# Performance work log

Hardware: AMD Instinct MI355X
Metric: run time of the kernel (lower is better)

The kernel has to match this reference:

```python
import jax, jax.numpy as jnp
import numpy as np

QUERY_INDS = (0, 1, 2, 3)
HEADS = 8
HEAD_DIM = 64
SCALE = HEAD_DIM ** -0.5
DIM = 512
INNER = HEADS * HEAD_DIM  # 512


def setup_inputs() -> dict:
    key = jax.random.key(0)
    ks = jax.random.split(key, 6)
    B, N = 4, 2048
    x = jax.random.normal(ks[0], (B, N, DIM), dtype=jnp.float32)
    bias = jax.random.normal(ks[1], (B, HEADS, N, N), dtype=jnp.float32)
    # weights stored as (in, out); math-equivalent to torch Linear
    Wq = jax.random.normal(ks[2], (DIM, INNER), dtype=jnp.float32) * (DIM ** -0.5)
    Wkv = jax.random.normal(ks[3], (DIM, 2 * INNER), dtype=jnp.float32) * (DIM ** -0.5)
    Wo = jax.random.normal(ks[4], (INNER, DIM), dtype=jnp.float32) * (INNER ** -0.5)
    bo = jax.random.normal(ks[5], (DIM,), dtype=jnp.float32) * 0.01
    return {"x": x, "bias": bias, "Wq": Wq, "Wkv": Wkv, "Wo": Wo, "bo": bo}


def _split_heads(t):
    # (B, n, H*d) -> (B, H, n, d)
    B, n, _ = t.shape
    return t.reshape(B, n, HEADS, HEAD_DIM).transpose(0, 2, 1, 3)


def reference(x, bias, Wq, Wkv, Wo, bo):
    qi = jnp.array(QUERY_INDS)
    q = _split_heads(x[:, qi] @ Wq)          # (B, H, M, d), M = len(QUERY_INDS)
    kv = x @ Wkv                              # (B, N, 2*inner)
    k, v = jnp.split(kv, 2, axis=-1)
    k = _split_heads(k)                       # (B, H, N, d)
    v = _split_heads(v)                       # (B, H, N, d)
    dots = jnp.einsum('bhmd,bhnd->bhmn', q, k) * SCALE
    dots = dots + bias[:, :, qi]              # gather bias rows at query positions
    attn = jax.nn.softmax(dots, axis=-1)      # dropout=0 (eval)
    out = jnp.einsum('bhmn,bhnd->bhmd', attn, v)
    B, _, M, _ = out.shape
    out = out.transpose(0, 2, 1, 3).reshape(B, M, INNER)  # (B, M, H*d)
    return out @ Wo + bo
```

## Files before the change

### kernel.cpp

```cpp
#include <hip/hip_runtime.h>
#include <stddef.h>

#define B_ 4
#define N_ 2048
#define C_ 512
#define H_ 8
#define D_ 64
#define M_ 4
#define HM_ 32
#define SCALE_ 0.125f

#define QK_OFF   0
#define DOTS_OFF 65536
#define AXP_OFF  (65536 + 524288)
#define Q_OFF    1114112
#define OV_OFF   1122304

__global__ __launch_bounds__(256) void zero_kernel(float* __restrict__ wsz, float* __restrict__ out) {
    int idx = blockIdx.x * 256 + threadIdx.x;
    if (idx < 16384) wsz[idx] = 0.f;
    else out[idx - 16384] = 0.f;
}

__global__ __launch_bounds__(256) void k1a_q(const float* __restrict__ x, const float* __restrict__ Wq,
                                             float* __restrict__ q_ws) {
    __shared__ float W[64][68];
    __shared__ float xr[16][68];
    int t = threadIdx.x;
    int c0 = blockIdx.x * 64, j0 = blockIdx.y * 64;
    #pragma unroll
    for (int i = 0; i < 4; i++) {
        int f = t + i * 256; int cc = f >> 4, j4 = f & 15;
        *(float4*)&W[cc][j4 * 4] = *(const float4*)&Wq[(size_t)(c0 + cc) * 512 + j0 + j4 * 4];
    }
    {
        int r = t >> 4, c4 = t & 15;
        int b = r >> 2, m = r & 3;
        *(float4*)&xr[r][c4 * 4] = *(const float4*)&x[((size_t)(b * N_) + m) * C_ + c0 + c4 * 4];
    }
    __syncthreads();
    int j = t & 63, rg = t >> 6;
    float acc[4] = {0, 0, 0, 0};
    #pragma unroll 16
    for (int cc = 0; cc < 64; cc++) {
        float w = W[cc][j];
        #pragma unroll
        for (int i = 0; i < 4; i++) acc[i] += xr[rg * 4 + i][cc] * w;
    }
    #pragma unroll
    for (int i = 0; i < 4; i++) {
        int r = rg * 4 + i;
        atomicAdd(&q_ws[r * 512 + j0 + j], acc[i]);
    }
}

__global__ __launch_bounds__(256) void k1b_qk(const float* __restrict__ Wkv, const float* __restrict__ q_ws,
                                              float* __restrict__ qk_ws) {
    __shared__ float WkT[64][68];
    __shared__ float qh[16][68];
    int t = threadIdx.x;
    int c0 = blockIdx.x * 64; int h = blockIdx.y;
    #pragma unroll
    for (int i = 0; i < 4; i++) {
        int f = t + i * 256; int cc = f >> 4, d4 = f & 15;
        float4 v = *(const float4*)&Wkv[(size_t)(c0 + cc) * 1024 + h * 64 + d4 * 4];
        WkT[d4 * 4 + 0][cc] = v.x; WkT[d4 * 4 + 1][cc] = v.y;
        WkT[d4 * 4 + 2][cc] = v.z; WkT[d4 * 4 + 3][cc] = v.w;
    }
    {
        int r = t >> 4, d4 = t & 15;
        *(float4*)&qh[r][d4 * 4] = *(const float4*)&q_ws[r * 512 + h * 64 + d4 * 4];
    }
    __syncthreads();
    int c = t & 63, rg = t >> 6;
    float acc[4] = {0, 0, 0, 0};
    #pragma unroll 16
    for (int d = 0; d < 64; d++) {
        float w = WkT[d][c];
        #pragma unroll
        for (int i = 0; i < 4; i++) acc[i] += qh[rg * 4 + i][d] * w;
    }
    #pragma unroll
    for (int i = 0; i < 4; i++) {
        int r = rg * 4 + i; int b = r >> 2, m = r & 3;
        qk_ws[((size_t)(b * HM_) + h * M_ + m) * 512 + c0 + c] = acc[i] * SCALE_;
    }
}

__global__ __launch_bounds__(256) void k2_dots(const float* __restrict__ x, const float* __restrict__ qk_ws,
                                               float* __restrict__ dots) {
    __shared__ float xt[64][66];
    __shared__ float qT[64][36];
    int t = threadIdx.x;
    int n0 = blockIdx.x * 64; int b = blockIdx.y; int ks = blockIdx.z;
    int p = t & 31, qg = t >> 5;
    float acc[2][4] = {{0, 0, 0, 0}, {0, 0, 0, 0}};
    for (int ch = 0; ch < 4; ch++) {
        int c0 = ks * 256 + ch * 64;
        #pragma unroll
        for (int i = 0; i < 4; i++) {
            int f = t + i * 256; int n = f >> 4, c4 = f & 15;
            float4 v = *(const float4*)&x[((size_t)(b * N_) + n0 + n) * C_ + c0 + c4 * 4];
            xt[c4 * 4 + 0][n] = v.x; xt[c4 * 4 + 1][n] = v.y;
            xt[c4 * 4 + 2][n] = v.z; xt[c4 * 4 + 3][n] = v.w;
        }
        #pragma unroll
        for (int i = 0; i < 2; i++) {
            int f = t + i * 256; int hm = f >> 4, c4 = f & 15;
            float4 v = *(const float4*)&qk_ws[((size_t)(b * HM_) + hm) * 512 + c0 + c4 * 4];
            qT[c4 * 4 + 0][hm] = v.x; qT[c4 * 4 + 1][hm] = v.y;
            qT[c4 * 4 + 2][hm] = v.z; qT[c4 * 4 + 3][hm] = v.w;
        }
        __syncthreads();
        #pragma unroll 16
        for (int kk = 0; kk < 64; kk++) {
            float2 xv = *(const float2*)&xt[kk][p * 2];
            float4 qv = *(const float4*)&qT[kk][qg * 4];
            acc[0][0] += qv.x * xv.x; acc[1][0] += qv.x * xv.y;
            acc[0][1] += qv.y * xv.x; acc[1][1] += qv.y * xv.y;
            acc[0][2] += qv.z * xv.x; acc[1][2] += qv.z * xv.y;
            acc[0][3] += qv.w * xv.x; acc[1][3] += qv.w * xv.y;
        }
        __syncthreads();
    }
    #pragma unroll
    for (int i = 0; i < 4; i++) {
        int hm = qg * 4 + i;
        *(float2*)&dots[(size_t)ks * 262144 + ((size_t)(b * HM_) + hm) * N_ + n0 + p * 2] =
            make_float2(acc[0][i], acc[1][i]);
    }
}

__global__ __launch_bounds__(256) void k3_softmax(const float* __restrict__ bias, float* __restrict__ dots) {
    __shared__ float red[256];
    int t = threadIdx.x;
    int row = blockIdx.x;
    int b = row >> 5, hm = row & 31, h = hm >> 2, m = hm & 3;
    const float* dA = dots + (size_t)row * N_;
    const float* dB = dots + 262144 + (size_t)row * N_;
    const float* brow = bias + ((size_t)(b * H_ + h) * N_ + m) * N_;
    float v[8];
    float mx = -1e30f;
    #pragma unroll
    for (int i = 0; i < 8; i++) {
        int n = t + i * 256;
        v[i] = dA[n] + dB[n] + brow[n];
        mx = fmaxf(mx, v[i]);
    }
    red[t] = mx; __syncthreads();
    for (int s = 128; s > 0; s >>= 1) { if (t < s) red[t] = fmaxf(red[t], red[t + s]); __syncthreads(); }
    mx = red[0]; __syncthreads();
    float ssum = 0.f;
    #pragma unroll
    for (int i = 0; i < 8; i++) { v[i] = __expf(v[i] - mx); ssum += v[i]; }
    red[t] = ssum; __syncthreads();
    for (int s = 128; s > 0; s >>= 1) { if (t < s) red[t] += red[t + s]; __syncthreads(); }
    float inv = 1.0f / red[0];
    float* aw = dots + (size_t)row * N_;
    #pragma unroll
    for (int i = 0; i < 8; i++) aw[t + i * 256] = v[i] * inv;
}

__global__ __launch_bounds__(256) void k4_attnx(const float* __restrict__ x, const float* __restrict__ attn,
                                                float* __restrict__ axp) {
    __shared__ float xn[64][68];
    __shared__ float at[64][36];
    int t = threadIdx.x;
    int c0 = blockIdx.x * 64; int s = blockIdx.y; int b = blockIdx.z;
    int p = t & 31, qg = t >> 5;
    float acc[2][4] = {{0, 0, 0, 0}, {0, 0, 0, 0}};
    for (int sub = 0; sub < 4; sub++) {
        int n0 = s * 256 + sub * 64;
        #pragma unroll
        for (int i = 0; i < 4; i++) {
            int f = t + i * 256; int nn = f >> 4, c4 = f & 15;
            *(float4*)&xn[nn][c4 * 4] =
                *(const float4*)&x[((size_t)(b * N_) + n0 + nn) * C_ + c0 + c4 * 4];
        }
        #pragma unroll
        for (int i = 0; i < 2; i++) {
            int f = t + i * 256; int hm = f >> 4, n4 = f & 15;
            float4 v = *(const float4*)&attn[((size_t)(b * HM_) + hm) * N_ + n0 + n4 * 4];
            at[n4 * 4 + 0][hm] = v.x; at[n4 * 4 + 1][hm] = v.y;
            at[n4 * 4 + 2][hm] = v.z; at[n4 * 4 + 3][hm] = v.w;
        }
        __syncthreads();
        #pragma unroll 16
        for (int nn = 0; nn < 64; nn++) {
            float2 xv = *(const float2*)&xn[nn][p * 2];
            float4 av = *(const float4*)&at[nn][qg * 4];
            acc[0][0] += av.x * xv.x; acc[1][0] += av.x * xv.y;
            acc[0][1] += av.y * xv.x; acc[1][1] += av.y * xv.y;
            acc[0][2] += av.z * xv.x; acc[1][2] += av.z * xv.y;
            acc[0][3] += av.w * xv.x; acc[1][3] += av.w * xv.y;
        }
        __syncthreads();
    }
    #pragma unroll
    for (int i = 0; i < 4; i++) {
        int hm = qg * 4 + i;
        *(float2*)&axp[(((size_t)(s * B_) + b) * HM_ + hm) * C_ + c0 + p * 2] =
            make_float2(acc[0][i], acc[1][i]);
    }
}

__global__ __launch_bounds__(256) void k5a_ov(const float* __restrict__ Wkv, const float* __restrict__ axp,
                                              float* __restrict__ ov_ws) {
    __shared__ float Wv[64][68];
    __shared__ float axh[16][68];
    int t = threadIdx.x;
    int c0 = blockIdx.x * 64; int h = blockIdx.y;
    #pragma unroll
    for (int i = 0; i < 4; i++) {
        int f = t + i * 256; int cc = f >> 4, e4 = f & 15;
        *(float4*)&Wv[cc][e4 * 4] =
            *(const float4*)&Wkv[(size_t)(c0 + cc) * 1024 + 512 + h * 64 + e4 * 4];
    }
    {
        int r = t >> 4, c4 = t & 15;
        int b = r >> 2, m = r & 3;
        float4 a = make_float4(0, 0, 0, 0);
        #pragma unroll
        for (int s = 0; s < 8; s++) {
            float4 v = *(const float4*)&axp[(((size_t)(s * B_) + b) * HM_ + h * M_ + m) * C_ + c0 + c4 * 4];
            a.x += v.x; a.y += v.y; a.z += v.z; a.w += v.w;
        }
        *(float4*)&axh[r][c4 * 4] = a;
    }
    __syncthreads();
    int e = t & 63, rg = t >> 6;
    float acc[4] = {0, 0, 0, 0};
    #pragma unroll 16
    for (int cc = 0; cc < 64; cc++) {
        float w = Wv[cc][e];
        #pragma unroll
        for (int i = 0; i < 4; i++) acc[i] += axh[rg * 4 + i][cc] * w;
    }
    #pragma unroll
    for (int i = 0; i < 4; i++) {
        int r = rg * 4 + i;
        atomicAdd(&ov_ws[r * 512 + h * 64 + e], acc[i]);
    }
}

__global__ __launch_bounds__(256) void k5b_out(const float* __restrict__ Wo, const float* __restrict__ bo,
                                               const float* __restrict__ ov_ws, float* __restrict__ out) {
    __shared__ float W[64][68];
    __shared__ float ovr[16][68];
    int t = threadIdx.x;
    int i0 = blockIdx.x * 64; int j0 = blockIdx.y * 64;
    #pragma unroll
    for (int i = 0; i < 4; i++) {
        int f = t + i * 256; int ii = f >> 4, j4 = f & 15;
        *(float4*)&W[ii][j4 * 4] = *(const float4*)&Wo[(size_t)(i0 + ii) * 512 + j0 + j4 * 4];
    }
    {
        int r = t >> 4, c4 = t & 15;
        *(float4*)&ovr[r][c4 * 4] = *(const float4*)&ov_ws[r * 512 + i0 + c4 * 4];
    }
    __syncthreads();
    int j = t & 63, rg = t >> 6;
    float binit = (blockIdx.x == 0) ? bo[j0 + j] : 0.f;
    float acc[4] = {binit, binit, binit, binit};
    #pragma unroll 16
    for (int ii = 0; ii < 64; ii++) {
        float w = W[ii][j];
        #pragma unroll
        for (int i = 0; i < 4; i++) acc[i] += ovr[rg * 4 + i][ii] * w;
    }
    #pragma unroll
    for (int i = 0; i < 4; i++) {
        int r = rg * 4 + i;
        atomicAdd(&out[r * 512 + j0 + j], acc[i]);
    }
}

extern "C" void kernel_launch(void* const* d_in, const int* in_sizes, int n_in,
                              void* d_out, int out_size, void* d_ws, size_t ws_size,
                              hipStream_t stream) {
    const float* x    = (const float*)d_in[0];
    const float* bias = (const float*)d_in[1];
    const float* Wq   = (const float*)d_in[2];
    const float* Wkv  = (const float*)d_in[3];
    const float* Wo   = (const float*)d_in[4];
    const float* bo   = (const float*)d_in[5];
    float* out = (float*)d_out;
    float* ws  = (float*)d_ws;

    float* qk_ws = ws + QK_OFF;
    float* dots  = ws + DOTS_OFF;
    float* axp   = ws + AXP_OFF;
    float* q_ws  = ws + Q_OFF;
    float* ov_ws = ws + OV_OFF;

    zero_kernel<<<96, 256, 0, stream>>>(q_ws, out);
    k1a_q<<<dim3(8, 8), 256, 0, stream>>>(x, Wq, q_ws);
    k1b_qk<<<dim3(8, 8), 256, 0, stream>>>(Wkv, q_ws, qk_ws);
    k2_dots<<<dim3(32, 4, 2), 256, 0, stream>>>(x, qk_ws, dots);
    k3_softmax<<<128, 256, 0, stream>>>(bias, dots);
    k4_attnx<<<dim3(8, 8, 4), 256, 0, stream>>>(x, dots, axp);
    k5a_ov<<<dim3(8, 8), 256, 0, stream>>>(Wkv, axp, ov_ws);
    k5b_out<<<dim3(8, 8), 256, 0, stream>>>(Wo, bo, ov_ws, out);
}
```

Before: 622.1 us.

## Enlarge register tiles to 4x4 in dots and attn-x kernels with finer split-K

The dots and attention-times-x kernels now give each thread a 4x4 output tile instead of 2x4, reading float4 from shared memory with wider 128-column tiles. The reduction dimension is split into more partitions (4 channel splits for dots, 16 sequence splits for attn-x) so the block count stays the same. Softmax and the output projection are updated to sum the extra partial buffers, and the workspace offsets grow to hold them. The goal is more FMAs per shared-memory load in these two GEMM-like stages, paid for with extra partial-sum traffic and larger workspace.

```diff
diff --git a/kernel.cpp b/kernel.cpp
--- a/kernel.cpp
+++ b/kernel.cpp
@@ -12,9 +12,9 @@
 
 #define QK_OFF   0
 #define DOTS_OFF 65536
-#define AXP_OFF  (65536 + 524288)
-#define Q_OFF    1114112
-#define OV_OFF   1122304
+#define AXP_OFF  (65536 + 1048576)
+#define Q_OFF    (65536 + 1048576 + 1048576)
+#define OV_OFF   (Q_OFF + 8192)
 
 __global__ __launch_bounds__(256) void zero_kernel(float* __restrict__ wsz, float* __restrict__ out) {
     int idx = blockIdx.x * 256 + threadIdx.x;
@@ -89,45 +89,47 @@
 
 __global__ __launch_bounds__(256) void k2_dots(const float* __restrict__ x, const float* __restrict__ qk_ws,
                                                float* __restrict__ dots) {
-    __shared__ float xt[64][66];
-    __shared__ float qT[64][36];
-    int t = threadIdx.x;
-    int n0 = blockIdx.x * 64; int b = blockIdx.y; int ks = blockIdx.z;
-    int p = t & 31, qg = t >> 5;
-    float acc[2][4] = {{0, 0, 0, 0}, {0, 0, 0, 0}};
-    for (int ch = 0; ch < 4; ch++) {
-        int c0 = ks * 256 + ch * 64;
-        #pragma unroll
-        for (int i = 0; i < 4; i++) {
-            int f = t + i * 256; int n = f >> 4, c4 = f & 15;
-            float4 v = *(const float4*)&x[((size_t)(b * N_) + n0 + n) * C_ + c0 + c4 * 4];
-            xt[c4 * 4 + 0][n] = v.x; xt[c4 * 4 + 1][n] = v.y;
-            xt[c4 * 4 + 2][n] = v.z; xt[c4 * 4 + 3][n] = v.w;
+    __shared__ __align__(16) float xt[64][132];
+    __shared__ __align__(16) float qT[64][36];
+    int t = threadIdx.x;
+    int n0 = blockIdx.x * 128; int b = blockIdx.y; int ks = blockIdx.z;
+    int p = t & 31, g = t >> 5;
+    float acc[4][4] = {{0,0,0,0},{0,0,0,0},{0,0,0,0},{0,0,0,0}};
+    for (int ch = 0; ch < 2; ch++) {
+        int cs = ks * 128 + ch * 64;
+        #pragma unroll
+        for (int it = 0; it < 8; it++) {
+            int cc = (t & 15) + 16 * (it & 3);
+            int q  = (t >> 4) + 16 * (it >> 2);
+            const float* gp = &x[((size_t)(b * N_) + n0 + 4 * q) * C_ + cs + cc];
+            float4 v;
+            v.x = gp[0]; v.y = gp[C_]; v.z = gp[2 * C_]; v.w = gp[3 * C_];
+            *(float4*)&xt[cc][4 * q] = v;
         }
         #pragma unroll
         for (int i = 0; i < 2; i++) {
             int f = t + i * 256; int hm = f >> 4, c4 = f & 15;
-            float4 v = *(const float4*)&qk_ws[((size_t)(b * HM_) + hm) * 512 + c0 + c4 * 4];
+            float4 v = *(const float4*)&qk_ws[((size_t)(b * HM_) + hm) * 512 + cs + c4 * 4];
             qT[c4 * 4 + 0][hm] = v.x; qT[c4 * 4 + 1][hm] = v.y;
             qT[c4 * 4 + 2][hm] = v.z; qT[c4 * 4 + 3][hm] = v.w;
         }
         __syncthreads();
-        #pragma unroll 16
+        #pragma unroll 8
         for (int kk = 0; kk < 64; kk++) {
-            float2 xv = *(const float2*)&xt[kk][p * 2];
-            float4 qv = *(const float4*)&qT[kk][qg * 4];
-            acc[0][0] += qv.x * xv.x; acc[1][0] += qv.x * xv.y;
-            acc[0][1] += qv.y * xv.x; acc[1][1] += qv.y * xv.y;
-            acc[0][2] += qv.z * xv.x; acc[1][2] += qv.z * xv.y;
-            acc[0][3] += qv.w * xv.x; acc[1][3] += qv.w * xv.y;
+            float4 xv = *(const float4*)&xt[kk][p * 4];
+            float4 qv = *(const float4*)&qT[kk][g * 4];
+            acc[0][0] += qv.x * xv.x; acc[0][1] += qv.x * xv.y; acc[0][2] += qv.x * xv.z; acc[0][3] += qv.x * xv.w;
+            acc[1][0] += qv.y * xv.x; acc[1][1] += qv.y * xv.y; acc[1][2] += qv.y * xv.z; acc[1][3] += qv.y * xv.w;
+            acc[2][0] += qv.z * xv.x; acc[2][1] += qv.z * xv.y; acc[2][2] += qv.z * xv.z; acc[2][3] += qv.z * xv.w;
+            acc[3][0] += qv.w * xv.x; acc[3][1] += qv.w * xv.y; acc[3][2] += qv.w * xv.z; acc[3][3] += qv.w * xv.w;
         }
         __syncthreads();
     }
     #pragma unroll
     for (int i = 0; i < 4; i++) {
-        int hm = qg * 4 + i;
-        *(float2*)&dots[(size_t)ks * 262144 + ((size_t)(b * HM_) + hm) * N_ + n0 + p * 2] =
-            make_float2(acc[0][i], acc[1][i]);
+        int hm = g * 4 + i;
+        *(float4*)&dots[(size_t)ks * 262144 + ((size_t)(b * HM_) + hm) * N_ + n0 + p * 4] =
+            make_float4(acc[i][0], acc[i][1], acc[i][2], acc[i][3]);
     }
 }
 
@@ -136,15 +138,17 @@
     int t = threadIdx.x;
     int row = blockIdx.x;
     int b = row >> 5, hm = row & 31, h = hm >> 2, m = hm & 3;
-    const float* dA = dots + (size_t)row * N_;
-    const float* dB = dots + 262144 + (size_t)row * N_;
+    const float* d0 = dots + (size_t)row * N_;
+    const float* d1 = dots + 262144 + (size_t)row * N_;
+    const float* d2 = dots + 524288 + (size_t)row * N_;
+    const float* d3 = dots + 786432 + (size_t)row * N_;
     const float* brow = bias + ((size_t)(b * H_ + h) * N_ + m) * N_;
     float v[8];
     float mx = -1e30f;
     #pragma unroll
     for (int i = 0; i < 8; i++) {
         int n = t + i * 256;
-        v[i] = dA[n] + dB[n] + brow[n];
+        v[i] = d0[n] + d1[n] + d2[n] + d3[n] + brow[n];
         mx = fmaxf(mx, v[i]);
     }
     red[t] = mx; __syncthreads();
@@ -163,19 +167,19 @@
 
 __global__ __launch_bounds__(256) void k4_attnx(const float* __restrict__ x, const float* __restrict__ attn,
                                                 float* __restrict__ axp) {
-    __shared__ float xn[64][68];
-    __shared__ float at[64][36];
-    int t = threadIdx.x;
-    int c0 = blockIdx.x * 64; int s = blockIdx.y; int b = blockIdx.z;
-    int p = t & 31, qg = t >> 5;
-    float acc[2][4] = {{0, 0, 0, 0}, {0, 0, 0, 0}};
-    for (int sub = 0; sub < 4; sub++) {
-        int n0 = s * 256 + sub * 64;
-        #pragma unroll
-        for (int i = 0; i < 4; i++) {
-            int f = t + i * 256; int nn = f >> 4, c4 = f & 15;
-            *(float4*)&xn[nn][c4 * 4] =
-                *(const float4*)&x[((size_t)(b * N_) + n0 + nn) * C_ + c0 + c4 * 4];
+    __shared__ __align__(16) float xn[64][132];
+    __shared__ __align__(16) float at[64][36];
+    int t = threadIdx.x;
+    int c0 = blockIdx.x * 128; int s = blockIdx.y; int b = blockIdx.z;
+    int p = t & 31, g = t >> 5;
+    float acc[4][4] = {{0,0,0,0},{0,0,0,0},{0,0,0,0},{0,0,0,0}};
+    for (int sub = 0; sub < 2; sub++) {
+        int n0 = s * 128 + sub * 64;
+        #pragma unroll
+        for (int i = 0; i < 8; i++) {
+            int f = t + i * 256; int nn = f >> 5, c8 = f & 31;
+            *(float4*)&xn[nn][c8 * 4] =
+                *(const float4*)&x[((size_t)(b * N_) + n0 + nn) * C_ + c0 + c8 * 4];
         }
         #pragma unroll
         for (int i = 0; i < 2; i++) {
@@ -185,22 +189,22 @@
             at[n4 * 4 + 2][hm] = v.z; at[n4 * 4 + 3][hm] = v.w;
         }
         __syncthreads();
-        #pragma unroll 16
+        #pragma unroll 8
         for (int nn = 0; nn < 64; nn++) {
-            float2 xv = *(const float2*)&xn[nn][p * 2];
-            float4 av = *(const float4*)&at[nn][qg * 4];
-            acc[0][0] += av.x * xv.x; acc[1][0] += av.x * xv.y;
-            acc[0][1] += av.y * xv.x; acc[1][1] += av.y * xv.y;
-            acc[0][2] += av.z * xv.x; acc[1][2] += av.z * xv.y;
-            acc[0][3] += av.w * xv.x; acc[1][3] += av.w * xv.y;
+            float4 xv = *(const float4*)&xn[nn][p * 4];
+            float4 av = *(const float4*)&at[nn][g * 4];
+            acc[0][0] += av.x * xv.x; acc[0][1] += av.x * xv.y; acc[0][2] += av.x * xv.z; acc[0][3] += av.x * xv.w;
+            acc[1][0] += av.y * xv.x; acc[1][1] += av.y * xv.y; acc[1][2] += av.y * xv.z; acc[1][3] += av.y * xv.w;
+            acc[2][0] += av.z * xv.x; acc[2][1] += av.z * xv.y; acc[2][2] += av.z * xv.z; acc[2][3] += av.z * xv.w;
+            acc[3][0] += av.w * xv.x; acc[3][1] += av.w * xv.y; acc[3][2] += av.w * xv.z; acc[3][3] += av.w * xv.w;
         }
         __syncthreads();
     }
     #pragma unroll
     for (int i = 0; i < 4; i++) {
-        int hm = qg * 4 + i;
-        *(float2*)&axp[(((size_t)(s * B_) + b) * HM_ + hm) * C_ + c0 + p * 2] =
-            make_float2(acc[0][i], acc[1][i]);
+        int hm = g * 4 + i;
+        *(float4*)&axp[(((size_t)(s * B_) + b) * HM_ + hm) * C_ + c0 + p * 4] =
+            make_float4(acc[i][0], acc[i][1], acc[i][2], acc[i][3]);
     }
 }
 
@@ -221,7 +225,7 @@
         int b = r >> 2, m = r & 3;
         float4 a = make_float4(0, 0, 0, 0);
         #pragma unroll
-        for (int s = 0; s < 8; s++) {
+        for (int s = 0; s < 16; s++) {
             float4 v = *(const float4*)&axp[(((size_t)(s * B_) + b) * HM_ + h * M_ + m) * C_ + c0 + c4 * 4];
             a.x += v.x; a.y += v.y; a.z += v.z; a.w += v.w;
         }
@@ -296,9 +300,9 @@
     zero_kernel<<<96, 256, 0, stream>>>(q_ws, out);
     k1a_q<<<dim3(8, 8), 256, 0, stream>>>(x, Wq, q_ws);
     k1b_qk<<<dim3(8, 8), 256, 0, stream>>>(Wkv, q_ws, qk_ws);
-    k2_dots<<<dim3(32, 4, 2), 256, 0, stream>>>(x, qk_ws, dots);
+    k2_dots<<<dim3(16, 4, 4), 256, 0, stream>>>(x, qk_ws, dots);
     k3_softmax<<<128, 256, 0, stream>>>(bias, dots);
-    k4_attnx<<<dim3(8, 8, 4), 256, 0, stream>>>(x, dots, axp);
+    k4_attnx<<<dim3(4, 16, 4), 256, 0, stream>>>(x, dots, axp);
     k5a_ov<<<dim3(8, 8), 256, 0, stream>>>(Wkv, axp, ov_ws);
     k5b_out<<<dim3(8, 8), 256, 0, stream>>>(Wo, bo, ov_ws, out);
 }
```

Result: no change. 615.8 us (-1.0%).

## Fuse dots, softmax and attn-x into flash-style split-N kernel with partial reductions

Applied to the files above, without the earlier changes.

Merges the dots, softmax and attention-times-x kernels into one kernel. Each block handles 32 keys for one batch and keeps a local max and sum. The combine step moves into k5a_ov, which rescales 64 partial results with the merged max and sum. The atomicAdd accumulations and the separate zero kernel are replaced by partial-sum buffers reduced in the following kernel, and zeroing of out moves into k1b_qk. This removes the dots round trip through global memory and several launches, but grows the partial workspace to 64 splits and leaves k5a_ov with a serial 64-step reduction.

```diff
diff --git a/kernel.cpp b/kernel.cpp
--- a/kernel.cpp
+++ b/kernel.cpp
@@ -8,22 +8,18 @@
 #define D_ 64
 #define M_ 4
 #define HM_ 32
+#define S_ 64
 #define SCALE_ 0.125f
 
 #define QK_OFF   0
-#define DOTS_OFF 65536
-#define AXP_OFF  (65536 + 524288)
-#define Q_OFF    1114112
-#define OV_OFF   1122304
-
-__global__ __launch_bounds__(256) void zero_kernel(float* __restrict__ wsz, float* __restrict__ out) {
-    int idx = blockIdx.x * 256 + threadIdx.x;
-    if (idx < 16384) wsz[idx] = 0.f;
-    else out[idx - 16384] = 0.f;
-}
+#define PAX_OFF  65536
+#define MLOC_OFF (65536 + 4194304)
+#define LLOC_OFF (MLOC_OFF + 8192)
+#define QP_OFF   (LLOC_OFF + 8192)
+#define OVP_OFF  (QP_OFF + 65536)
 
 __global__ __launch_bounds__(256) void k1a_q(const float* __restrict__ x, const float* __restrict__ Wq,
-                                             float* __restrict__ q_ws) {
+                                             float* __restrict__ q_part) {
     __shared__ float W[64][68];
     __shared__ float xr[16][68];
     int t = threadIdx.x;
@@ -50,16 +46,18 @@
     #pragma unroll
     for (int i = 0; i < 4; i++) {
         int r = rg * 4 + i;
-        atomicAdd(&q_ws[r * 512 + j0 + j], acc[i]);
-    }
-}
-
-__global__ __launch_bounds__(256) void k1b_qk(const float* __restrict__ Wkv, const float* __restrict__ q_ws,
-                                              float* __restrict__ qk_ws) {
+        q_part[((size_t)blockIdx.x * 16 + r) * 512 + j0 + j] = acc[i];
+    }
+}
+
+__global__ __launch_bounds__(256) void k1b_qk(const float* __restrict__ Wkv, const float* __restrict__ q_part,
+                                              float* __restrict__ qk_ws, float* __restrict__ out) {
     __shared__ float WkT[64][68];
     __shared__ float qh[16][68];
     int t = threadIdx.x;
     int c0 = blockIdx.x * 64; int h = blockIdx.y;
+    int bid = blockIdx.y * 8 + blockIdx.x;
+    if (bid < 32) out[bid * 256 + t] = 0.f;
     #pragma unroll
     for (int i = 0; i < 4; i++) {
         int f = t + i * 256; int cc = f >> 4, d4 = f & 15;
@@ -69,7 +67,13 @@
     }
     {
         int r = t >> 4, d4 = t & 15;
-        *(float4*)&qh[r][d4 * 4] = *(const float4*)&q_ws[r * 512 + h * 64 + d4 * 4];
+        float4 a = make_float4(0.f, 0.f, 0.f, 0.f);
+        #pragma unroll
+        for (int cs = 0; cs < 8; cs++) {
+            float4 v = *(const float4*)&q_part[((size_t)cs * 16 + r) * 512 + h * 64 + d4 * 4];
+            a.x += v.x; a.y += v.y; a.z += v.z; a.w += v.w;
+        }
+        *(float4*)&qh[r][d4 * 4] = a;
     }
     __syncthreads();
     int c = t & 63, rg = t >> 6;
@@ -87,127 +91,170 @@
     }
 }
 
-__global__ __launch_bounds__(256) void k2_dots(const float* __restrict__ x, const float* __restrict__ qk_ws,
-                                               float* __restrict__ dots) {
-    __shared__ float xt[64][66];
-    __shared__ float qT[64][36];
-    int t = threadIdx.x;
-    int n0 = blockIdx.x * 64; int b = blockIdx.y; int ks = blockIdx.z;
-    int p = t & 31, qg = t >> 5;
-    float acc[2][4] = {{0, 0, 0, 0}, {0, 0, 0, 0}};
-    for (int ch = 0; ch < 4; ch++) {
-        int c0 = ks * 256 + ch * 64;
-        #pragma unroll
-        for (int i = 0; i < 4; i++) {
-            int f = t + i * 256; int n = f >> 4, c4 = f & 15;
-            float4 v = *(const float4*)&x[((size_t)(b * N_) + n0 + n) * C_ + c0 + c4 * 4];
-            xt[c4 * 4 + 0][n] = v.x; xt[c4 * 4 + 1][n] = v.y;
-            xt[c4 * 4 + 2][n] = v.z; xt[c4 * 4 + 3][n] = v.w;
-        }
-        #pragma unroll
-        for (int i = 0; i < 2; i++) {
-            int f = t + i * 256; int hm = f >> 4, c4 = f & 15;
-            float4 v = *(const float4*)&qk_ws[((size_t)(b * HM_) + hm) * 512 + c0 + c4 * 4];
-            qT[c4 * 4 + 0][hm] = v.x; qT[c4 * 4 + 1][hm] = v.y;
-            qT[c4 * 4 + 2][hm] = v.z; qT[c4 * 4 + 3][hm] = v.w;
-        }
-        __syncthreads();
-        #pragma unroll 16
-        for (int kk = 0; kk < 64; kk++) {
-            float2 xv = *(const float2*)&xt[kk][p * 2];
-            float4 qv = *(const float4*)&qT[kk][qg * 4];
-            acc[0][0] += qv.x * xv.x; acc[1][0] += qv.x * xv.y;
-            acc[0][1] += qv.y * xv.x; acc[1][1] += qv.y * xv.y;
-            acc[0][2] += qv.z * xv.x; acc[1][2] += qv.z * xv.y;
-            acc[0][3] += qv.w * xv.x; acc[1][3] += qv.w * xv.y;
-        }
-        __syncthreads();
-    }
-    #pragma unroll
-    for (int i = 0; i < 4; i++) {
-        int hm = qg * 4 + i;
-        *(float2*)&dots[(size_t)ks * 262144 + ((size_t)(b * HM_) + hm) * N_ + n0 + p * 2] =
-            make_float2(acc[0][i], acc[1][i]);
-    }
-}
-
-__global__ __launch_bounds__(256) void k3_softmax(const float* __restrict__ bias, float* __restrict__ dots) {
-    __shared__ float red[256];
-    int t = threadIdx.x;
-    int row = blockIdx.x;
-    int b = row >> 5, hm = row & 31, h = hm >> 2, m = hm & 3;
-    const float* dA = dots + (size_t)row * N_;
-    const float* dB = dots + 262144 + (size_t)row * N_;
-    const float* brow = bias + ((size_t)(b * H_ + h) * N_ + m) * N_;
-    float v[8];
-    float mx = -1e30f;
+__global__ __launch_bounds__(256) void k234_flash(const float* __restrict__ x, const float* __restrict__ qk_ws,
+                                                  const float* __restrict__ bias,
+                                                  float* __restrict__ pax, float* __restrict__ mloc,
+                                                  float* __restrict__ lloc) {
+    __shared__ __align__(16) float qk_s[32][516];
+    __shared__ __align__(16) float scratch[4][32][32];
+    __shared__ __align__(16) float dmat[32][36];
+    __shared__ __align__(16) float pT[32][36];
+    __shared__ float mrow[32];
+    __shared__ float red8[32][8];
+    int t = threadIdx.x;
+    int s = blockIdx.x, b = blockIdx.y;
+    int n0 = s * 32;
+
+    #pragma unroll
+    for (int k = 0; k < 16; k++) {
+        int idx = t + k * 256;
+        int row = idx >> 7, c4 = idx & 127;
+        *(float4*)&qk_s[row][c4 * 4] =
+            *(const float4*)&qk_ws[((size_t)(b * HM_) + row) * 512 + c4 * 4];
+    }
+    __syncthreads();
+
+    int hmg = t >> 6;
+    int ng  = (t >> 3) & 7;
+    int cs  = t & 7;
+    float d[8][4];
+    #pragma unroll
+    for (int i = 0; i < 8; i++)
+        #pragma unroll
+        for (int jn = 0; jn < 4; jn++) d[i][jn] = 0.f;
+
+    const float* xp = &x[((size_t)(b * N_) + n0 + ng * 4) * C_];
+    const float* qrow = &qk_s[hmg * 8][0];
+    #pragma unroll 2
+    for (int step = 0; step < 16; step++) {
+        int cbase = cs * 4 + step * 32;
+        float4 xv[4];
+        #pragma unroll
+        for (int jn = 0; jn < 4; jn++)
+            xv[jn] = *(const float4*)&xp[(size_t)jn * C_ + cbase];
+        #pragma unroll
+        for (int i = 0; i < 8; i++) {
+            float4 qv = *(const float4*)&qrow[i * 516 + cbase];
+            #pragma unroll
+            for (int jn = 0; jn < 4; jn++) {
+                d[i][jn] += qv.x * xv[jn].x + qv.y * xv[jn].y + qv.z * xv[jn].z + qv.w * xv[jn].w;
+            }
+        }
+    }
+    int pos = hmg * 8 + ng;
+    if (cs >= 4) {
+        #pragma unroll
+        for (int i = 0; i < 8; i++)
+            *(float4*)&scratch[cs - 4][pos][i * 4] = make_float4(d[i][0], d[i][1], d[i][2], d[i][3]);
+    }
+    __syncthreads();
+    if (cs < 4) {
+        #pragma unroll
+        for (int i = 0; i < 8; i++) {
+            float4 v = *(float4*)&scratch[cs][pos][i * 4];
+            d[i][0] += v.x; d[i][1] += v.y; d[i][2] += v.z; d[i][3] += v.w;
+        }
+    }
+    __syncthreads();
+    if (cs == 2 || cs == 3) {
+        #pragma unroll
+        for (int i = 0; i < 8; i++)
+            *(float4*)&scratch[cs - 2][pos][i * 4] = make_float4(d[i][0], d[i][1], d[i][2], d[i][3]);
+    }
+    __syncthreads();
+    if (cs < 2) {
+        #pragma unroll
+        for (int i = 0; i < 8; i++) {
+            float4 v = *(float4*)&scratch[cs][pos][i * 4];
+            d[i][0] += v.x; d[i][1] += v.y; d[i][2] += v.z; d[i][3] += v.w;
+        }
+    }
+    __syncthreads();
+    if (cs == 1) {
+        #pragma unroll
+        for (int i = 0; i < 8; i++)
+            *(float4*)&scratch[0][pos][i * 4] = make_float4(d[i][0], d[i][1], d[i][2], d[i][3]);
+    }
+    __syncthreads();
+    if (cs == 0) {
+        #pragma unroll
+        for (int i = 0; i < 8; i++) {
+            float4 v = *(float4*)&scratch[0][pos][i * 4];
+            *(float4*)&dmat[hmg * 8 + i][ng * 4] =
+                make_float4(d[i][0] + v.x, d[i][1] + v.y, d[i][2] + v.z, d[i][3] + v.w);
+        }
+    }
+    __syncthreads();
+
+    int row = t >> 3, j = t & 7;
+    int h = row >> 2, m = row & 3;
+    float4 dv = *(float4*)&dmat[row][j * 4];
+    float4 bv = *(const float4*)&bias[(((size_t)(b * H_) + h) * N_ + m) * N_ + n0 + j * 4];
+    float v0 = dv.x + bv.x, v1 = dv.y + bv.y, v2 = dv.z + bv.z, v3 = dv.w + bv.w;
+    float pmax = fmaxf(fmaxf(v0, v1), fmaxf(v2, v3));
+    red8[row][j] = pmax;
+    __syncthreads();
+    if (j == 0) {
+        float mg = red8[row][0];
+        #pragma unroll
+        for (int k = 1; k < 8; k++) mg = fmaxf(mg, red8[row][k]);
+        mrow[row] = mg;
+    }
+    __syncthreads();
+    float mg = mrow[row];
+    float e0 = __expf(v0 - mg), e1 = __expf(v1 - mg), e2 = __expf(v2 - mg), e3 = __expf(v3 - mg);
+    red8[row][j] = e0 + e1 + e2 + e3;
+    __syncthreads();
+    if (j == 0) {
+        float ls = red8[row][0];
+        #pragma unroll
+        for (int k = 1; k < 8; k++) ls += red8[row][k];
+        mloc[((size_t)(s * B_) + b) * HM_ + row] = mg;
+        lloc[((size_t)(s * B_) + b) * HM_ + row] = ls;
+    }
+    pT[j * 4 + 0][row] = e0; pT[j * 4 + 1][row] = e1;
+    pT[j * 4 + 2][row] = e2; pT[j * 4 + 3][row] = e3;
+    __syncthreads();
+
+    int cg = t & 63, hw = t >> 6;
+    float o[8][8];
+    #pragma unroll
+    for (int i = 0; i < 8; i++)
+        #pragma unroll
+        for (int jj = 0; jj < 8; jj++) o[i][jj] = 0.f;
+    const float* xb = &x[((size_t)(b * N_) + n0) * C_];
+    #pragma unroll 4
+    for (int n = 0; n < 32; n++) {
+        float4 pa = *(float4*)&pT[n][hw * 8];
+        float4 pb = *(float4*)&pT[n][hw * 8 + 4];
+        float4 xa = *(const float4*)&xb[(size_t)n * C_ + cg * 4];
+        float4 xc = *(const float4*)&xb[(size_t)n * C_ + 256 + cg * 4];
+        float pv[8] = {pa.x, pa.y, pa.z, pa.w, pb.x, pb.y, pb.z, pb.w};
+        #pragma unroll
+        for (int i = 0; i < 8; i++) {
+            o[i][0] += pv[i] * xa.x; o[i][1] += pv[i] * xa.y;
+            o[i][2] += pv[i] * xa.z; o[i][3] += pv[i] * xa.w;
+            o[i][4] += pv[i] * xc.x; o[i][5] += pv[i] * xc.y;
+            o[i][6] += pv[i] * xc.z; o[i][7] += pv[i] * xc.w;
+        }
+    }
     #pragma unroll
     for (int i = 0; i < 8; i++) {
-        int n = t + i * 256;
-        v[i] = dA[n] + dB[n] + brow[n];
-        mx = fmaxf(mx, v[i]);
-    }
-    red[t] = mx; __syncthreads();
-    for (int s = 128; s > 0; s >>= 1) { if (t < s) red[t] = fmaxf(red[t], red[t + s]); __syncthreads(); }
-    mx = red[0]; __syncthreads();
-    float ssum = 0.f;
-    #pragma unroll
-    for (int i = 0; i < 8; i++) { v[i] = __expf(v[i] - mx); ssum += v[i]; }
-    red[t] = ssum; __syncthreads();
-    for (int s = 128; s > 0; s >>= 1) { if (t < s) red[t] += red[t + s]; __syncthreads(); }
-    float inv = 1.0f / red[0];
-    float* aw = dots + (size_t)row * N_;
-    #pragma unroll
-    for (int i = 0; i < 8; i++) aw[t + i * 256] = v[i] * inv;
-}
-
-__global__ __launch_bounds__(256) void k4_attnx(const float* __restrict__ x, const float* __restrict__ attn,
-                                                float* __restrict__ axp) {
-    __shared__ float xn[64][68];
-    __shared__ float at[64][36];
-    int t = threadIdx.x;
-    int c0 = blockIdx.x * 64; int s = blockIdx.y; int b = blockIdx.z;
-    int p = t & 31, qg = t >> 5;
-    float acc[2][4] = {{0, 0, 0, 0}, {0, 0, 0, 0}};
-    for (int sub = 0; sub < 4; sub++) {
-        int n0 = s * 256 + sub * 64;
-        #pragma unroll
-        for (int i = 0; i < 4; i++) {
-            int f = t + i * 256; int nn = f >> 4, c4 = f & 15;
-            *(float4*)&xn[nn][c4 * 4] =
-                *(const float4*)&x[((size_t)(b * N_) + n0 + nn) * C_ + c0 + c4 * 4];
-        }
-        #pragma unroll
-        for (int i = 0; i < 2; i++) {
-            int f = t + i * 256; int hm = f >> 4, n4 = f & 15;
-            float4 v = *(const float4*)&attn[((size_t)(b * HM_) + hm) * N_ + n0 + n4 * 4];
-            at[n4 * 4 + 0][hm] = v.x; at[n4 * 4 + 1][hm] = v.y;
-            at[n4 * 4 + 2][hm] = v.z; at[n4 * 4 + 3][hm] = v.w;
-        }
-        __syncthreads();
-        #pragma unroll 16
-        for (int nn = 0; nn < 64; nn++) {
-            float2 xv = *(const float2*)&xn[nn][p * 2];
-            float4 av = *(const float4*)&at[nn][qg * 4];
-            acc[0][0] += av.x * xv.x; acc[1][0] += av.x * xv.y;
-            acc[0][1] += av.y * xv.x; acc[1][1] += av.y * xv.y;
-            acc[0][2] += av.z * xv.x; acc[1][2] += av.z * xv.y;
-            acc[0][3] += av.w * xv.x; acc[1][3] += av.w * xv.y;
-        }
-        __syncthreads();
-    }
-    #pragma unroll
-    for (int i = 0; i < 4; i++) {
-        int hm = qg * 4 + i;
-        *(float2*)&axp[(((size_t)(s * B_) + b) * HM_ + hm) * C_ + c0 + p * 2] =
-            make_float2(acc[0][i], acc[1][i]);
-    }
-}
-
-__global__ __launch_bounds__(256) void k5a_ov(const float* __restrict__ Wkv, const float* __restrict__ axp,
-                                              float* __restrict__ ov_ws) {
+        int hm = hw * 8 + i;
+        float* dst = &pax[(((size_t)(s * B_) + b) * HM_ + hm) * 512];
+        *(float4*)&dst[cg * 4]       = make_float4(o[i][0], o[i][1], o[i][2], o[i][3]);
+        *(float4*)&dst[256 + cg * 4] = make_float4(o[i][4], o[i][5], o[i][6], o[i][7]);
+    }
+}
+
+__global__ __launch_bounds__(256) void k5a_ov(const float* __restrict__ Wkv, const float* __restrict__ pax,
+                                              const float* __restrict__ mloc, const float* __restrict__ lloc,
+                                              float* __restrict__ ov_part) {
     __shared__ float Wv[64][68];
     __shared__ float axh[16][68];
+    __shared__ float sc[64][16];
+    __shared__ float redm[16][16];
+    __shared__ float mgl[16], lgl[16];
     int t = threadIdx.x;
     int c0 = blockIdx.x * 64; int h = blockIdx.y;
     #pragma unroll
@@ -216,16 +263,55 @@
         *(float4*)&Wv[cc][e4 * 4] =
             *(const float4*)&Wkv[(size_t)(c0 + cc) * 1024 + 512 + h * 64 + e4 * 4];
     }
+    int r = t & 15, sg = t >> 4;
+    int b = r >> 2, m = r & 3;
+    float pm = -1e30f;
+    #pragma unroll
+    for (int k = 0; k < 4; k++) {
+        int s = sg * 4 + k;
+        pm = fmaxf(pm, mloc[((size_t)(s * B_) + b) * HM_ + h * M_ + m]);
+    }
+    redm[sg][r] = pm;
+    __syncthreads();
+    if (t < 16) {
+        float mg = redm[0][t];
+        #pragma unroll
+        for (int k = 1; k < 16; k++) mg = fmaxf(mg, redm[k][t]);
+        mgl[t] = mg;
+    }
+    __syncthreads();
+    float mg = mgl[r];
+    float pl = 0.f;
+    #pragma unroll
+    for (int k = 0; k < 4; k++) {
+        int s = sg * 4 + k;
+        float w = __expf(mloc[((size_t)(s * B_) + b) * HM_ + h * M_ + m] - mg);
+        sc[s][r] = w;
+        pl += w * lloc[((size_t)(s * B_) + b) * HM_ + h * M_ + m];
+    }
+    redm[sg][r] = pl;
+    __syncthreads();
+    if (t < 16) {
+        float l = redm[0][t];
+        #pragma unroll
+        for (int k = 1; k < 16; k++) l += redm[k][t];
+        lgl[t] = 1.0f / l;
+    }
+    __syncthreads();
+    float inv = lgl[r];
+    #pragma unroll
+    for (int k = 0; k < 4; k++) sc[sg * 4 + k][r] *= inv;
+    __syncthreads();
     {
-        int r = t >> 4, c4 = t & 15;
-        int b = r >> 2, m = r & 3;
-        float4 a = make_float4(0, 0, 0, 0);
-        #pragma unroll
-        for (int s = 0; s < 8; s++) {
-            float4 v = *(const float4*)&axp[(((size_t)(s * B_) + b) * HM_ + h * M_ + m) * C_ + c0 + c4 * 4];
-            a.x += v.x; a.y += v.y; a.z += v.z; a.w += v.w;
-        }
-        *(float4*)&axh[r][c4 * 4] = a;
+        int rr = t >> 4, c4 = t & 15;
+        int bb = rr >> 2, mm = rr & 3;
+        float4 a = make_float4(0.f, 0.f, 0.f, 0.f);
+        for (int s = 0; s < 64; s++) {
+            float w = sc[s][rr];
+            float4 v = *(const float4*)&pax[(((size_t)(s * B_) + bb) * HM_ + h * M_ + mm) * 512 + c0 + c4 * 4];
+            a.x += w * v.x; a.y += w * v.y; a.z += w * v.z; a.w += w * v.w;
+        }
+        *(float4*)&axh[rr][c4 * 4] = a;
     }
     __syncthreads();
     int e = t & 63, rg = t >> 6;
@@ -238,13 +324,13 @@
     }
     #pragma unroll
     for (int i = 0; i < 4; i++) {
-        int r = rg * 4 + i;
-        atomicAdd(&ov_ws[r * 512 + h * 64 + e], acc[i]);
+        int rr = rg * 4 + i;
+        ov_part[((size_t)blockIdx.x * 16 + rr) * 512 + h * 64 + e] = acc[i];
     }
 }
 
 __global__ __launch_bounds__(256) void k5b_out(const float* __restrict__ Wo, const float* __restrict__ bo,
-                                               const float* __restrict__ ov_ws, float* __restrict__ out) {
+                                               const float* __restrict__ ov_part, float* __restrict__ out) {
     __shared__ float W[64][68];
     __shared__ float ovr[16][68];
     int t = threadIdx.x;
@@ -256,7 +342,13 @@
     }
     {
         int r = t >> 4, c4 = t & 15;
-        *(float4*)&ovr[r][c4 * 4] = *(const float4*)&ov_ws[r * 512 + i0 + c4 * 4];
+        float4 a = make_float4(0.f, 0.f, 0.f, 0.f);
+        #pragma unroll
+        for (int cs = 0; cs < 8; cs++) {
+            float4 v = *(const float4*)&ov_part[((size_t)cs * 16 + r) * 512 + i0 + c4 * 4];
+            a.x += v.x; a.y += v.y; a.z += v.z; a.w += v.w;
+        }
+        *(float4*)&ovr[r][c4 * 4] = a;
     }
     __syncthreads();
     int j = t & 63, rg = t >> 6;
@@ -287,18 +379,16 @@
     float* out = (float*)d_out;
     float* ws  = (float*)d_ws;
 
-    float* qk_ws = ws + QK_OFF;
-    float* dots  = ws + DOTS_OFF;
-    float* axp   = ws + AXP_OFF;
-    float* q_ws  = ws + Q_OFF;
-    float* ov_ws = ws + OV_OFF;
-
-    zero_kernel<<<96, 256, 0, stream>>>(q_ws, out);
-    k1a_q<<<dim3(8, 8), 256, 0, stream>>>(x, Wq, q_ws);
-    k1b_qk<<<dim3(8, 8), 256, 0, stream>>>(Wkv, q_ws, qk_ws);
-    k2_dots<<<dim3(32, 4, 2), 256, 0, stream>>>(x, qk_ws, dots);
-    k3_softmax<<<128, 256, 0, stream>>>(bias, dots);
-    k4_attnx<<<dim3(8, 8, 4), 256, 0, stream>>>(x, dots, axp);
-    k5a_ov<<<dim3(8, 8), 256, 0, stream>>>(Wkv, axp, ov_ws);
-    k5b_out<<<dim3(8, 8), 256, 0, stream>>>(Wo, bo, ov_ws, out);
-}
+    float* qk_ws   = ws + QK_OFF;
+    float* pax     = ws + PAX_OFF;
+    float* mloc    = ws + MLOC_OFF;
+    float* lloc    = ws + LLOC_OFF;
+    float* q_part  = ws + QP_OFF;
+    float* ov_part = ws + OVP_OFF;
+
+    k1a_q<<<dim3(8, 8), 256, 0, stream>>>(x, Wq, q_part);
+    k1b_qk<<<dim3(8, 8), 256, 0, stream>>>(Wkv, q_part, qk_ws, out);
+    k234_flash<<<dim3(S_, B_), 256, 0, stream>>>(x, qk_ws, bias, pax, mloc, lloc);
+    k5a_ov<<<dim3(8, 8), 256, 0, stream>>>(Wkv, pax, mloc, lloc, ov_part);
+    k5b_out<<<dim3(8, 8), 256, 0, stream>>>(Wo, bo, ov_part, out);
+}
```

New measurement: 609.8 us. -2.0%, faster.
